# Optimization experiments

Measured on AMD Instinct MI355X. Metric: run time of the kernel, lower is better.

The kernel has to match this reference:

```python
import jax, jax.numpy as jnp
import numpy as np

B, NQ, NKV, D, H, E, FF = 2, 1024, 2048, 1024, 16, 8, 4096
DH = D // H


def _ln(x, g, b):
    m = x.mean(-1, keepdims=True)
    v = ((x - m) ** 2).mean(-1, keepdims=True)
    return (x - m) / jnp.sqrt(v + 1e-5) * g + b


def _mha(q, kv, in_w, in_b, out_w, out_b):
    # torch nn.MultiheadAttention, batch_first=True, dropout=0 (eval)
    wq, wk, wv = jnp.split(in_w, 3, axis=0)   # each [D, D]
    bq, bk, bv = jnp.split(in_b, 3)
    qp = q @ wq.T + bq
    kp = kv @ wk.T + bk
    vp = kv @ wv.T + bv

    def heads(x):
        b, t, _ = x.shape
        return x.reshape(b, t, H, DH).transpose(0, 2, 1, 3)  # [b,H,t,DH]

    qh, kh, vh = heads(qp), heads(kp), heads(vp)
    scores = jnp.einsum('bhqd,bhkd->bhqk', qh, kh) / jnp.sqrt(jnp.float32(DH))
    att = jax.nn.softmax(scores, axis=-1)
    o = jnp.einsum('bhqk,bhkd->bhqd', att, vh)
    o = o.transpose(0, 2, 1, 3).reshape(q.shape[0], q.shape[1], D)
    return o @ out_w.T + out_b


def _moe_token(x, rw, rb, nw, nb, w1, b1, w2, b2, top_k, key):
    # SparseMoE_token: per-token noisy top-k routing.
    logits = x @ rw.T + rb                      # [B,T,E]
    noise_logits = x @ nw.T + nb
    noise = jax.random.normal(key, logits.shape, logits.dtype) * jax.nn.softplus(noise_logits)
    noisy = logits + noise
    _, idx = jax.lax.top_k(noisy, top_k)        # [B,T,K]
    mask = jax.nn.one_hot(idx, E, dtype=noisy.dtype).sum(-2) > 0   # [B,T,E]
    probs = jax.nn.softmax(jnp.where(mask, noisy, -jnp.inf), axis=-1)
    # Dense expert compute weighted by sparse router probs (zeros for
    # non-selected experts) — math identical to masked gather/scatter.
    h = jax.nn.gelu(jnp.einsum('btd,edh->beth', x, w1) + b1[None, :, None, :],
                    approximate=False)          # [B,E,T,FF]
    eo = jnp.einsum('beth,ehd->betd', h, w2) + b2[None, :, None, :]
    return jnp.einsum('bte,betd->btd', probs, eo)


def reference(q, kv,
              ln_cq_g, ln_cq_b, ln_ckv_g, ln_ckv_b, ln_s_g, ln_s_b, ln_m_g, ln_m_b,
              ca_in_w, ca_in_b, ca_out_w, ca_out_b,
              sa_in_w, sa_in_b, sa_out_w, sa_out_b,
              moe_rw, moe_rb, moe_nw, moe_nb, moe_w1, moe_b1, moe_w2, moe_b2,
              top_k):
    key = jax.random.key(42)
    x = _mha(_ln(q, ln_cq_g, ln_cq_b), _ln(kv, ln_ckv_g, ln_ckv_b),
             ca_in_w, ca_in_b, ca_out_w, ca_out_b) + q
    xs = _ln(x, ln_s_g, ln_s_b)
    x = _mha(xs, xs, sa_in_w, sa_in_b, sa_out_w, sa_out_b) + x
    x = _moe_token(_ln(x, ln_m_g, ln_m_b), moe_rw, moe_rb, moe_nw, moe_nb,
                   moe_w1, moe_b1, moe_w2, moe_b2, top_k, key) + x
    return x


def setup_inputs() -> dict:
    key = jax.random.key(0)
    ks = jax.random.split(key, 16)
    s = 0.02
    return {
        'q':  jax.random.normal(ks[0], (B, NQ, D), jnp.float32),
        'kv': jax.random.normal(ks[1], (B, NKV, D), jnp.float32),
        'ln_cq_g': jnp.ones((D,), jnp.float32),  'ln_cq_b': jnp.zeros((D,), jnp.float32),
        'ln_ckv_g': jnp.ones((D,), jnp.float32), 'ln_ckv_b': jnp.zeros((D,), jnp.float32),
        'ln_s_g': jnp.ones((D,), jnp.float32),   'ln_s_b': jnp.zeros((D,), jnp.float32),
        'ln_m_g': jnp.ones((D,), jnp.float32),   'ln_m_b': jnp.zeros((D,), jnp.float32),
        'ca_in_w':  jax.random.normal(ks[2], (3 * D, D), jnp.float32) * s,
        'ca_in_b':  jnp.zeros((3 * D,), jnp.float32),
        'ca_out_w': jax.random.normal(ks[3], (D, D), jnp.float32) * s,
        'ca_out_b': jnp.zeros((D,), jnp.float32),
        'sa_in_w':  jax.random.normal(ks[4], (3 * D, D), jnp.float32) * s,
        'sa_in_b':  jnp.zeros((3 * D,), jnp.float32),
        'sa_out_w': jax.random.normal(ks[5], (D, D), jnp.float32) * s,
        'sa_out_b': jnp.zeros((D,), jnp.float32),
        'moe_rw': jax.random.normal(ks[6], (E, D), jnp.float32) * s,
        'moe_rb': jnp.zeros((E,), jnp.float32),
        'moe_nw': jax.random.normal(ks[7], (E, D), jnp.float32) * s,
        'moe_nb': jnp.zeros((E,), jnp.float32),
        'moe_w1': jax.random.normal(ks[8], (E, D, FF), jnp.float32) * s,
        'moe_b1': jnp.zeros((E, FF), jnp.float32),
        'moe_w2': jax.random.normal(ks[9], (E, FF, D), jnp.float32) * s,
        'moe_b2': jnp.zeros((E, D), jnp.float32),
        'top_k': 2,
    }
```

## Files before the change

### kernel.cpp

```cpp
#include <hip/hip_runtime.h>
#include <cstdint>
#include <cstddef>

#define JAX_THREEFRY_PARTITIONABLE 1

typedef unsigned short u16;
typedef unsigned int u32;
typedef __attribute__((ext_vector_type(8))) short bf16x8;
typedef __attribute__((ext_vector_type(4))) float f32x4;

struct Ptr8 { u16* p[8]; };

struct QkvArgs {
  const u16* ah[3]; const u16* al[3];
  const u16* wh[3]; const u16* wl[3];
  const float* bias[3];
  float* c[3];
  int M[3];
};

__device__ __forceinline__ int imin_(int a, int b) { return a < b ? a : b; }

__device__ __forceinline__ u16 f2bf_(float f) {
  unsigned u = __float_as_uint(f);
  return (u16)((u + 0x7fffu + ((u >> 16) & 1u)) >> 16);
}
__device__ __forceinline__ float bf2f_(u16 h) {
  return __uint_as_float(((unsigned)h) << 16);
}

__device__ __forceinline__ void split2_(float a, float b, u32& hi, u32& lo) {
  u16 h0 = f2bf_(a), h1 = f2bf_(b);
  u16 l0 = f2bf_(a - bf2f_(h0)), l1 = f2bf_(b - bf2f_(h1));
  hi = (u32)h0 | ((u32)h1 << 16);
  lo = (u32)l0 | ((u32)l1 << 16);
}

union FragU {
  u32 w[4];
  uint4 q;
  bf16x8 v;
};

__device__ __forceinline__ unsigned rotl32_(unsigned v, int d) {
  return (v << d) | (v >> (32 - d));
}

__device__ __forceinline__ void threefry2x32_(unsigned k0, unsigned k1,
                                              unsigned x0, unsigned x1,
                                              unsigned& o0, unsigned& o1) {
  unsigned ks2 = k0 ^ k1 ^ 0x1BD11BDAu;
  x0 += k0; x1 += k1;
#define TF_R(rot) { x0 += x1; x1 = rotl32_(x1, rot); x1 ^= x0; }
  TF_R(13) TF_R(15) TF_R(26) TF_R(6)
  x0 += k1;  x1 += ks2 + 1u;
  TF_R(17) TF_R(29) TF_R(16) TF_R(24)
  x0 += ks2; x1 += k0 + 2u;
  TF_R(13) TF_R(15) TF_R(26) TF_R(6)
  x0 += k0;  x1 += k1 + 3u;
  TF_R(17) TF_R(29) TF_R(16) TF_R(24)
  x0 += k1;  x1 += ks2 + 4u;
  TF_R(13) TF_R(15) TF_R(26) TF_R(6)
  x0 += ks2; x1 += k0 + 5u;
#undef TF_R
  o0 = x0; o1 = x1;
}

__device__ float erfinv_f32_(float x) {
  float w = -log1pf(-x * x);
  float p;
  if (w < 5.0f) {
    w -= 2.5f;
    p = 2.81022636e-08f;
    p = fmaf(p, w, 3.43273939e-07f);
    p = fmaf(p, w, -3.5233877e-06f);
    p = fmaf(p, w, -4.39150654e-06f);
    p = fmaf(p, w, 0.00021858087f);
    p = fmaf(p, w, -0.00125372503f);
    p = fmaf(p, w, -0.00417768164f);
    p = fmaf(p, w, 0.246640727f);
    p = fmaf(p, w, 1.50140941f);
  } else {
    w = sqrtf(w) - 3.0f;
    p = -0.000200214257f;
    p = fmaf(p, w, 0.000100950558f);
    p = fmaf(p, w, 0.00134934322f);
    p = fmaf(p, w, -0.00367342844f);
    p = fmaf(p, w, 0.00573950773f);
    p = fmaf(p, w, -0.0076224613f);
    p = fmaf(p, w, 0.00943887047f);
    p = fmaf(p, w, 1.00167406f);
    p = fmaf(p, w, 2.83297682f);
  }
  return p * x;
}

__device__ float bits_to_normal_(unsigned b) {
  const float lo = -0.99999994f;
  float f = __uint_as_float((b >> 9) | 0x3f800000u) - 1.0f;
  float u = fmaxf(lo, f * 2.0f + lo);
  return 1.41421356237f * erfinv_f32_(u);
}

__global__ __launch_bounds__(256) void noise_kernel(float* __restrict__ normals) {
  int i = blockIdx.x * 256 + threadIdx.x;
#if JAX_THREEFRY_PARTITIONABLE
  if (i < 16384) {
    unsigned o0, o1;
    threefry2x32_(0u, 42u, 0u, (unsigned)i, o0, o1);
    normals[i] = bits_to_normal_(o0 ^ o1);
  }
#else
  if (i < 8192) {
    unsigned o0, o1;
    threefry2x32_(0u, 42u, (unsigned)i, (unsigned)(i + 8192), o0, o1);
    normals[i] = bits_to_normal_(o0);
    normals[i + 8192] = bits_to_normal_(o1);
  }
#endif
}

__device__ float block_reduce_sum_(float v) {
  for (int m = 1; m <= 32; m <<= 1) v += __shfl_xor(v, m, 64);
  __shared__ float red[4];
  int lane = threadIdx.x & 63, w = threadIdx.x >> 6;
  if (lane == 0) red[w] = v;
  __syncthreads();
  v = red[0] + red[1] + red[2] + red[3];
  __syncthreads();
  return v;
}

__global__ __launch_bounds__(256) void ln_kernel(
    const float* __restrict__ X, const float* __restrict__ g,
    const float* __restrict__ bta, float* __restrict__ Y) {
  int row = blockIdx.x;
  int t = threadIdx.x;
  const float4* xr = (const float4*)(X + (size_t)row * 1024);
  float4 v = xr[t];
  float s = v.x + v.y + v.z + v.w;
  s = block_reduce_sum_(s);
  float mean = s * (1.0f / 1024.0f);
  float dx = v.x - mean, dy = v.y - mean, dz = v.z - mean, dw = v.w - mean;
  float sq = dx * dx + dy * dy + dz * dz + dw * dw;
  sq = block_reduce_sum_(sq);
  float rstd = 1.0f / sqrtf(sq * (1.0f / 1024.0f) + 1e-5f);
  float4 gv = ((const float4*)g)[t];
  float4 bv = ((const float4*)bta)[t];
  float4 y;
  y.x = dx * rstd * gv.x + bv.x;
  y.y = dy * rstd * gv.y + bv.y;
  y.z = dz * rstd * gv.z + bv.z;
  y.w = dw * rstd * gv.w + bv.w;
  ((float4*)(Y + (size_t)row * 1024))[t] = y;
}

__global__ __launch_bounds__(256) void ln_split_kernel(
    const float* __restrict__ X, const float* __restrict__ g,
    const float* __restrict__ bta, u16* __restrict__ Yh,
    u16* __restrict__ Yl) {
  int row = blockIdx.x;
  int t = threadIdx.x;
  const float4* xr = (const float4*)(X + (size_t)row * 1024);
  float4 v = xr[t];
  float s = v.x + v.y + v.z + v.w;
  s = block_reduce_sum_(s);
  float mean = s * (1.0f / 1024.0f);
  float dx = v.x - mean, dy = v.y - mean, dz = v.z - mean, dw = v.w - mean;
  float sq = dx * dx + dy * dy + dz * dz + dw * dw;
  sq = block_reduce_sum_(sq);
  float rstd = 1.0f / sqrtf(sq * (1.0f / 1024.0f) + 1e-5f);
  float4 gv = ((const float4*)g)[t];
  float4 bv = ((const float4*)bta)[t];
  float y[4];
  y[0] = dx * rstd * gv.x + bv.x;
  y[1] = dy * rstd * gv.y + bv.y;
  y[2] = dz * rstd * gv.z + bv.z;
  y[3] = dw * rstd * gv.w + bv.w;
  ushort4 h, l;
  u16* hp = (u16*)&h; u16* lp = (u16*)&l;
#pragma unroll
  for (int j = 0; j < 4; ++j) {
    u16 hh = f2bf_(y[j]);
    hp[j] = hh;
    lp[j] = f2bf_(y[j] - bf2f_(hh));
  }
  *(ushort4*)(Yh + (size_t)row * 1024 + t * 4) = h;
  *(ushort4*)(Yl + (size_t)row * 1024 + t * 4) = l;
}

__global__ __launch_bounds__(256) void cvt_split_kernel(
    const float* __restrict__ src, u16* __restrict__ hi,
    u16* __restrict__ lo) {
  int i = (blockIdx.x * 256 + threadIdx.x) * 4;
  float4 v = *(const float4*)(src + i);
  float a[4] = {v.x, v.y, v.z, v.w};
  ushort4 h, l;
  u16* hp = (u16*)&h; u16* lp = (u16*)&l;
#pragma unroll
  for (int j = 0; j < 4; ++j) {
    u16 hh = f2bf_(a[j]);
    hp[j] = hh;
    lp[j] = f2bf_(a[j] - bf2f_(hh));
  }
  *(ushort4*)(hi + i) = h;
  *(ushort4*)(lo + i) = l;
}

__global__ __launch_bounds__(256) void tcvt_kernel(
    const float* __restrict__ src, Ptr8 dst, int R, int C) {
  __shared__ float tile[64][65];
  const int e = blockIdx.z;
  const float* S = src + (size_t)e * R * C;
  u16* D = dst.p[e];
  const int c0 = blockIdx.x * 64, r0 = blockIdx.y * 64;
  const int t = threadIdx.x;
  const int tr = t >> 4, tc = (t & 15) * 4;
#pragma unroll
  for (int p = 0; p < 4; ++p) {
    float4 v = *(const float4*)(S + (size_t)(r0 + p * 16 + tr) * C + c0 + tc);
    tile[p * 16 + tr][tc + 0] = v.x;
    tile[p * 16 + tr][tc + 1] = v.y;
    tile[p * 16 + tr][tc + 2] = v.z;
    tile[p * 16 + tr][tc + 3] = v.w;
  }
  __syncthreads();
#pragma unroll
  for (int p = 0; p < 4; ++p) {
    int oc = p * 16 + tr;
    ushort4 o;
    o.x = f2bf_(tile[tc + 0][oc]);
    o.y = f2bf_(tile[tc + 1][oc]);
    o.z = f2bf_(tile[tc + 2][oc]);
    o.w = f2bf_(tile[tc + 3][oc]);
    *(ushort4*)(D + (size_t)(c0 + oc) * R + r0 + tc) = o;
  }
}

template<bool RESID>
__device__ __forceinline__ void split_gemm_body_(
    const u16* __restrict__ Ah, const u16* __restrict__ Al,
    const u16* __restrict__ Wh, const u16* __restrict__ Wl,
    const float* __restrict__ bias, const float* __restrict__ resid,
    float* __restrict__ C, int m0, int n0, int N, int K) {
  __shared__ __align__(16) u16 Ahs[128 * 40];
  __shared__ __align__(16) u16 Als[128 * 40];
  __shared__ __align__(16) u16 Bhs[128 * 40];
  __shared__ __align__(16) u16 Bls[128 * 40];
  const int t = threadIdx.x;
  const int lane = t & 63, wv = t >> 6;
  const int wm = (wv & 1) * 64, wn = (wv >> 1) * 64;
  const int col = lane & 15, quad = lane >> 4;
  f32x4 acc[4][4] = {};
  const int r = t >> 1, kh = (t & 1) * 16;
  const u16* pah = Ah + (size_t)(m0 + r) * K + kh;
  const u16* pal = Al + (size_t)(m0 + r) * K + kh;
  const u16* pwh = Wh + (size_t)(n0 + r) * K + kh;
  const u16* pwl = Wl + (size_t)(n0 + r) * K + kh;
  uint4 ra0 = *(const uint4*)(pah), ra1 = *(const uint4*)(pah + 8);
  uint4 rb0 = *(const uint4*)(pal), rb1 = *(const uint4*)(pal + 8);
  uint4 rc0 = *(const uint4*)(pwh), rc1 = *(const uint4*)(pwh + 8);
  uint4 rd0 = *(const uint4*)(pwl), rd1 = *(const uint4*)(pwl + 8);
  for (int k0 = 0; k0 < K; k0 += 32) {
    pah += 32; pal += 32; pwh += 32; pwl += 32;
    *(uint4*)&Ahs[r * 40 + kh] = ra0; *(uint4*)&Ahs[r * 40 + kh + 8] = ra1;
    *(uint4*)&Als[r * 40 + kh] = rb0; *(uint4*)&Als[r * 40 + kh + 8] = rb1;
    *(uint4*)&Bhs[r * 40 + kh] = rc0; *(uint4*)&Bhs[r * 40 + kh + 8] = rc1;
    *(uint4*)&Bls[r * 40 + kh] = rd0; *(uint4*)&Bls[r * 40 + kh + 8] = rd1;
    __syncthreads();
    if (k0 + 32 < K) {
      ra0 = *(const uint4*)(pah); ra1 = *(const uint4*)(pah + 8);
      rb0 = *(const uint4*)(pal); rb1 = *(const uint4*)(pal + 8);
      rc0 = *(const uint4*)(pwh); rc1 = *(const uint4*)(pwh + 8);
      rd0 = *(const uint4*)(pwl); rd1 = *(const uint4*)(pwl + 8);
    }
    bf16x8 afh[4], afl[4], bfh[4], bfl[4];
#pragma unroll
    for (int i = 0; i < 4; ++i) {
      afh[i] = *(const bf16x8*)&Ahs[(wm + i * 16 + col) * 40 + quad * 8];
      afl[i] = *(const bf16x8*)&Als[(wm + i * 16 + col) * 40 + quad * 8];
    }
#pragma unroll
    for (int j = 0; j < 4; ++j) {
      bfh[j] = *(const bf16x8*)&Bhs[(wn + j * 16 + col) * 40 + quad * 8];
      bfl[j] = *(const bf16x8*)&Bls[(wn + j * 16 + col) * 40 + quad * 8];
    }
#pragma unroll
    for (int i = 0; i < 4; ++i) {
#pragma unroll
      for (int j = 0; j < 4; ++j) {
        acc[i][j] = __builtin_amdgcn_mfma_f32_16x16x32_bf16(afh[i], bfh[j], acc[i][j], 0, 0, 0);
        acc[i][j] = __builtin_amdgcn_mfma_f32_16x16x32_bf16(afh[i], bfl[j], acc[i][j], 0, 0, 0);
        acc[i][j] = __builtin_amdgcn_mfma_f32_16x16x32_bf16(afl[i], bfh[j], acc[i][j], 0, 0, 0);
      }
    }
    __syncthreads();
  }
  float bv[4];
#pragma unroll
  for (int j = 0; j < 4; ++j) bv[j] = bias[n0 + wn + j * 16 + col];
#pragma unroll
  for (int i = 0; i < 4; ++i) {
#pragma unroll
    for (int rr = 0; rr < 4; ++rr) {
      int m = m0 + wm + i * 16 + quad * 4 + rr;
      float* crow = C + (size_t)m * N;
      const float* rrow = RESID ? (resid + (size_t)m * N) : nullptr;
#pragma unroll
      for (int j = 0; j < 4; ++j) {
        int n = n0 + wn + j * 16 + col;
        float v = acc[i][j][rr] + bv[j];
        if (RESID) v += rrow[n];
        crow[n] = v;
      }
    }
  }
}

template<bool RESID>
__global__ __launch_bounds__(256) void split_gemm_nt(
    const u16* __restrict__ Ah, const u16* __restrict__ Al,
    const u16* __restrict__ Wh, const u16* __restrict__ Wl,
    const float* __restrict__ bias, const float* __restrict__ resid,
    float* __restrict__ C, int M, int N, int K) {
  (void)M;
  split_gemm_body_<RESID>(Ah, Al, Wh, Wl, bias, resid, C,
                          blockIdx.y * 128, blockIdx.x * 128, N, K);
}

__global__ __launch_bounds__(256) void split_gemm_qkv(QkvArgs a, int N, int K) {
  const int z = blockIdx.z;
  const int m0 = blockIdx.y * 128;
  if (m0 >= a.M[z]) return;
  split_gemm_body_<false>(a.ah[z], a.al[z], a.wh[z], a.wl[z], a.bias[z],
                          nullptr, a.c[z], m0, blockIdx.x * 128, N, K);
}

__global__ __launch_bounds__(256) void attn_kernel(
    const float* __restrict__ QP, const float* __restrict__ KP,
    const float* __restrict__ VP, u16* __restrict__ AOh,
    u16* __restrict__ AOl, int nq, int nkv) {
  __shared__ __align__(16) u16 Ksh[64 * 72];
  __shared__ __align__(16) u16 Ksl[64 * 72];
  __shared__ __align__(16) u16 Vth[64 * 72];
  __shared__ __align__(16) u16 Vtl[64 * 72];
  const int t = threadIdx.x;
  const int lane = t & 63, wv = t >> 6;
  const int col = lane & 15, quad = lane >> 4;
  const int bh = blockIdx.x;
  const int b = bh >> 4, h = bh & 15;
  const int q0 = blockIdx.y * 64;
  const int wq0 = wv * 16;

  bf16x8 qbh[2], qbl[2];
  {
    const float* qsrc =
        QP + (size_t)(b * nq + q0 + wq0 + col) * 1024 + h * 64 + quad * 8;
#pragma unroll
    for (int ks = 0; ks < 2; ++ks) {
      float4 f0 = *(const float4*)(qsrc + ks * 32);
      float4 f1 = *(const float4*)(qsrc + ks * 32 + 4);
      float qf[8] = {f0.x, f0.y, f0.z, f0.w, f1.x, f1.y, f1.z, f1.w};
      FragU uh, ul;
#pragma unroll
      for (int w = 0; w < 4; ++w)
        split2_(qf[2 * w] * 0.125f, qf[2 * w + 1] * 0.125f, uh.w[w], ul.w[w]);
      qbh[ks] = uh.v;
      qbl[ks] = ul.v;
    }
  }

  f32x4 o[4] = {};
  float mi = -INFINITY, li = 0.0f;

  const int kr = t >> 2, kc = (t & 3) * 16;
  const int vg = t >> 5, vr = (t & 31) * 2;

  for (int kv0 = 0; kv0 < nkv; kv0 += 64) {
    {
      const float* ksrc =
          KP + (size_t)(b * nkv + kv0 + kr) * 1024 + h * 64 + kc;
      float4 f0 = *(const float4*)(ksrc);
      float4 f1 = *(const float4*)(ksrc + 4);
      float4 f2 = *(const float4*)(ksrc + 8);
      float4 f3 = *(const float4*)(ksrc + 12);
      float kf[16] = {f0.x, f0.y, f0.z, f0.w, f1.x, f1.y, f1.z, f1.w,
                      f2.x, f2.y, f2.z, f2.w, f3.x, f3.y, f3.z, f3.w};
      FragU h0, h1, l0, l1;
#pragma unroll
      for (int w = 0; w < 4; ++w) {
        split2_(kf[2 * w], kf[2 * w + 1], h0.w[w], l0.w[w]);
        split2_(kf[8 + 2 * w], kf[9 + 2 * w], h1.w[w], l1.w[w]);
      }
      *(uint4*)&Ksh[kr * 72 + kc] = h0.q;
      *(uint4*)&Ksh[kr * 72 + kc + 8] = h1.q;
      *(uint4*)&Ksl[kr * 72 + kc] = l0.q;
      *(uint4*)&Ksl[kr * 72 + kc + 8] = l1.q;
    }
    {
      const float* vsrc =
          VP + (size_t)(b * nkv + kv0 + vr) * 1024 + h * 64 + vg * 8;
      float4 a0 = *(const float4*)(vsrc);
      float4 a1 = *(const float4*)(vsrc + 4);
      float4 b0 = *(const float4*)(vsrc + 1024);
      float4 b1 = *(const float4*)(vsrc + 1028);
      float va[8] = {a0.x, a0.y, a0.z, a0.w, a1.x, a1.y, a1.z, a1.w};
      float vb[8] = {b0.x, b0.y, b0.z, b0.w, b1.x, b1.y, b1.z, b1.w};
#pragma unroll
      for (int e = 0; e < 8; ++e) {
        u32 hh, ll;
        split2_(va[e], vb[e], hh, ll);
        *(u32*)&Vth[(vg * 8 + e) * 72 + vr] = hh;
        *(u32*)&Vtl[(vg * 8 + e) * 72 + vr] = ll;
      }
    }
    __syncthreads();

    f32x4 st[4] = {};
#pragma unroll
    for (int ks = 0; ks < 2; ++ks) {
      bf16x8 kah[4], kal[4];
#pragma unroll
      for (int i = 0; i < 4; ++i) {
        kah[i] = *(const bf16x8*)&Ksh[(i * 16 + col) * 72 + ks * 32 + quad * 8];
        kal[i] = *(const bf16x8*)&Ksl[(i * 16 + col) * 72 + ks * 32 + quad * 8];
      }
#pragma unroll
      for (int i = 0; i < 4; ++i) {
        st[i] = __builtin_amdgcn_mfma_f32_16x16x32_bf16(kah[i], qbh[ks], st[i], 0, 0, 0);
        st[i] = __builtin_amdgcn_mfma_f32_16x16x32_bf16(kah[i], qbl[ks], st[i], 0, 0, 0);
        st[i] = __builtin_amdgcn_mfma_f32_16x16x32_bf16(kal[i], qbh[ks], st[i], 0, 0, 0);
      }
    }

    float tmax = st[0][0];
#pragma unroll
    for (int i = 0; i < 4; ++i)
#pragma unroll
      for (int r = 0; r < 4; ++r) tmax = fmaxf(tmax, st[i][r]);
    tmax = fmaxf(tmax, __shfl_xor(tmax, 16, 64));
    tmax = fmaxf(tmax, __shfl_xor(tmax, 32, 64));
    float mnew = fmaxf(mi, tmax);
    float alpha = __expf(mi - mnew);
    float tsum = 0.0f;
#pragma unroll
    for (int i = 0; i < 4; ++i) {
#pragma unroll
      for (int r = 0; r < 4; ++r) {
        float p = __expf(st[i][r] - mnew);
        st[i][r] = p;
        tsum += p;
      }
    }
    tsum += __shfl_xor(tsum, 16, 64);
    tsum += __shfl_xor(tsum, 32, 64);
    li = li * alpha + tsum;
    mi = mnew;
    float alr[4];
#pragma unroll
    for (int r = 0; r < 4; ++r)
      alr[r] = __shfl(alpha, (lane & 48) | (quad * 4 + r), 64);
#pragma unroll
    for (int j = 0; j < 4; ++j)
#pragma unroll
      for (int r = 0; r < 4; ++r) o[j][r] *= alr[r];

    u32 pkh[4][2], pkl[4][2];
#pragma unroll
    for (int i = 0; i < 4; ++i)
#pragma unroll
      for (int w = 0; w < 2; ++w)
        split2_(st[i][2 * w], st[i][2 * w + 1], pkh[i][w], pkl[i][w]);
    u32 APh[2][4], APl[2][4];
    const int par = quad >> 1;
#pragma unroll
    for (int i = 0; i < 4; ++i) {
#pragma unroll
      for (int w01 = 0; w01 < 2; ++w01) {
#pragma unroll
        for (int dw = 0; dw < 2; ++dw) {
          int src = (((2 * quad + dw) & 3) << 4) | col;
          u32 vh = (u32)__shfl((int)pkh[i][w01], src, 64);
          u32 vl = (u32)__shfl((int)pkl[i][w01], src, 64);
          if ((i & 1) == par) {
            APh[i >> 1][dw * 2 + w01] = vh;
            APl[i >> 1][dw * 2 + w01] = vl;
          }
        }
      }
    }

#pragma unroll
    for (int ks = 0; ks < 2; ++ks) {
      FragU fh, fl;
#pragma unroll
      for (int w = 0; w < 4; ++w) { fh.w[w] = APh[ks][w]; fl.w[w] = APl[ks][w]; }
      bf16x8 pah = fh.v, pal = fl.v;
#pragma unroll
      for (int j = 0; j < 4; ++j) {
        bf16x8 vbh = *(const bf16x8*)&Vth[(j * 16 + col) * 72 + ks * 32 + quad * 8];
        bf16x8 vbl = *(const bf16x8*)&Vtl[(j * 16 + col) * 72 + ks * 32 + quad * 8];
        o[j] = __builtin_amdgcn_mfma_f32_16x16x32_bf16(pah, vbh, o[j], 0, 0, 0);
        o[j] = __builtin_amdgcn_mfma_f32_16x16x32_bf16(pah, vbl, o[j], 0, 0, 0);
        o[j] = __builtin_amdgcn_mfma_f32_16x16x32_bf16(pal, vbh, o[j], 0, 0, 0);
      }
    }
    __syncthreads();
  }

  float inv = 1.0f / li;
  float ivr[4];
#pragma unroll
  for (int r = 0; r < 4; ++r)
    ivr[r] = __shfl(inv, (lane & 48) | (quad * 4 + r), 64);
#pragma unroll
  for (int r = 0; r < 4; ++r) {
    size_t base =
        (size_t)(b * nq + q0 + wq0 + quad * 4 + r) * 1024 + h * 64 + col;
#pragma unroll
    for (int j = 0; j < 4; ++j) {
      float v = o[j][r] * ivr[r];
      u16 hh = f2bf_(v);
      AOh[base + j * 16] = hh;
      AOl[base + j * 16] = f2bf_(v - bf2f_(hh));
    }
  }
}

__global__ __launch_bounds__(256) void router_kernel(
    const float* __restrict__ xm, const float* __restrict__ rw,
    const float* __restrict__ rb, const float* __restrict__ nw,
    const float* __restrict__ nb, float* __restrict__ logits,
    float* __restrict__ nlogits) {
  int row = blockIdx.x, t = threadIdx.x;
  const float* x = xm + (size_t)row * 1024;
  float accl[8] = {}, accn[8] = {};
  for (int d = t; d < 1024; d += 256) {
    float xv = x[d];
#pragma unroll
    for (int e = 0; e < 8; ++e) {
      accl[e] += xv * rw[e * 1024 + d];
      accn[e] += xv * nw[e * 1024 + d];
    }
  }
  __shared__ float red[16][4];
  int lane = t & 63, w = t >> 6;
#pragma unroll
  for (int e = 0; e < 8; ++e) {
    float v = accl[e];
    for (int m = 1; m <= 32; m <<= 1) v += __shfl_xor(v, m, 64);
    if (lane == 0) red[e][w] = v;
    float v2 = accn[e];
    for (int m = 1; m <= 32; m <<= 1) v2 += __shfl_xor(v2, m, 64);
    if (lane == 0) red[8 + e][w] = v2;
  }
  __syncthreads();
  if (t < 8)
    logits[row * 8 + t] = red[t][0] + red[t][1] + red[t][2] + red[t][3] + rb[t];
  else if (t < 16)
    nlogits[row * 8 + t - 8] =
        red[t][0] + red[t][1] + red[t][2] + red[t][3] + nb[t - 8];
}

__global__ __launch_bounds__(256) void route_kernel(
    const float* __restrict__ logits, const float* __restrict__ nlogits,
    const float* __restrict__ normals, int* __restrict__ routei,
    float* __restrict__ routep, int* __restrict__ cnt) {
  int bt = blockIdx.x * 256 + threadIdx.x;
  if (bt >= 2048) return;
  float noisy[8];
#pragma unroll
  for (int e = 0; e < 8; ++e) {
    float nl = nlogits[bt * 8 + e];
    float sp = fmaxf(nl, 0.0f) + log1pf(expf(-fabsf(nl)));
    noisy[e] = logits[bt * 8 + e] + normals[bt * 8 + e] * sp;
  }
  int i1 = 0; float n1 = noisy[0];
#pragma unroll
  for (int e = 1; e < 8; ++e) if (noisy[e] > n1) { n1 = noisy[e]; i1 = e; }
  int i2 = -1; float n2 = -INFINITY;
#pragma unroll
  for (int e = 0; e < 8; ++e)
    if (e != i1 && noisy[e] > n2) { n2 = noisy[e]; i2 = e; }
  float e2 = expf(n2 - n1);
  float denom = 1.0f + e2;
  routei[bt * 2 + 0] = i1; routei[bt * 2 + 1] = i2;
  routep[bt * 2 + 0] = 1.0f / denom; routep[bt * 2 + 1] = e2 / denom;
  atomicAdd(&cnt[i1], 1);
  atomicAdd(&cnt[i2], 1);
}

__global__ void zero_kernel(int* __restrict__ cnt) {
  if (threadIdx.x < 8) cnt[threadIdx.x] = 0;
}

__global__ void offs_kernel(const int* __restrict__ cnt, int* __restrict__ offs,
                            int* __restrict__ fill) {
  if (threadIdx.x == 0 && blockIdx.x == 0) {
    int o = 0;
    for (int e = 0; e < 8; ++e) { offs[e] = o; o += cnt[e]; fill[e] = 0; }
  }
}

__global__ __launch_bounds__(256) void fill_kernel(
    const int* __restrict__ routei, const float* __restrict__ routep,
    const int* __restrict__ offs, int* __restrict__ fill,
    int* __restrict__ alist, float* __restrict__ aprob) {
  int bt = blockIdx.x * 256 + threadIdx.x;
  if (bt >= 2048) return;
#pragma unroll
  for (int s = 0; s < 2; ++s) {
    int e = routei[bt * 2 + s];
    int pos = offs[e] + atomicAdd(&fill[e], 1);
    alist[pos] = bt;
    aprob[pos] = routep[bt * 2 + s];
  }
}

__global__ __launch_bounds__(256) void copy_kernel(const float* __restrict__ src,
                                                   float* __restrict__ dst) {
  int i = blockIdx.x * 256 + threadIdx.x;
  ((float4*)dst)[i] = ((const float4*)src)[i];
}

__global__ __launch_bounds__(256) void f2bf_kernel(const float* __restrict__ src,
                                                   u16* __restrict__ dst) {
  int i = (blockIdx.x * 256 + threadIdx.x) * 4;
  float4 v = *(const float4*)(src + i);
  ushort4 o;
  o.x = f2bf_(v.x); o.y = f2bf_(v.y); o.z = f2bf_(v.z); o.w = f2bf_(v.w);
  *(ushort4*)(dst + i) = o;
}

__device__ __forceinline__ float gelu_exact_(float x) {
  return 0.5f * x * (1.0f + erff(x * 0.70710678f));
}

__global__ __launch_bounds__(256) void ffn1_mfma(
    const u16* __restrict__ Xb, Ptr8 w1t, const float* __restrict__ B1,
    u16* __restrict__ H, const int* __restrict__ alist,
    const int* __restrict__ cnt, const int* __restrict__ offs) {
  const int e = blockIdx.z;
  const int ce = cnt[e];
  const int m0 = blockIdx.y * 128;
  if (m0 >= ce) return;
  const int off = offs[e];
  const int n0 = blockIdx.x * 128;
  const u16* __restrict__ WT = w1t.p[e];
  __shared__ __align__(16) u16 As[128 * 40];
  __shared__ __align__(16) u16 Bs[128 * 40];
  const int t = threadIdx.x;
  const int lane = t & 63, wv = t >> 6;
  const int wm = (wv & 1) * 64, wn = (wv >> 1) * 64;
  const int col = lane & 15, quad = lane >> 4;
  f32x4 acc[4][4] = {};
  const int r = t >> 1, ak = (t & 1) * 16;
  const int arow = alist[off + imin_(m0 + r, ce - 1)];
  const u16* asrc = Xb + (size_t)arow * 1024 + ak;
  const u16* wsrc = WT + (size_t)(n0 + r) * 1024 + ak;
  uint4 ra0 = *(const uint4*)(asrc), ra1 = *(const uint4*)(asrc + 8);
  uint4 rb0 = *(const uint4*)(wsrc), rb1 = *(const uint4*)(wsrc + 8);
  for (int k0 = 0; k0 < 1024; k0 += 32) {
    asrc += 32; wsrc += 32;
    *(uint4*)&As[r * 40 + ak] = ra0; *(uint4*)&As[r * 40 + ak + 8] = ra1;
    *(uint4*)&Bs[r * 40 + ak] = rb0; *(uint4*)&Bs[r * 40 + ak + 8] = rb1;
    __syncthreads();
    if (k0 + 32 < 1024) {
      ra0 = *(const uint4*)(asrc); ra1 = *(const uint4*)(asrc + 8);
      rb0 = *(const uint4*)(wsrc); rb1 = *(const uint4*)(wsrc + 8);
    }
    bf16x8 af[4], bf[4];
#pragma unroll
    for (int i = 0; i < 4; ++i)
      af[i] = *(const bf16x8*)&As[(wm + i * 16 + col) * 40 + quad * 8];
#pragma unroll
    for (int j = 0; j < 4; ++j)
      bf[j] = *(const bf16x8*)&Bs[(wn + j * 16 + col) * 40 + quad * 8];
#pragma unroll
    for (int i = 0; i < 4; ++i)
#pragma unroll
      for (int j = 0; j < 4; ++j)
        acc[i][j] = __builtin_amdgcn_mfma_f32_16x16x32_bf16(af[i], bf[j], acc[i][j], 0, 0, 0);
    __syncthreads();
  }
#pragma unroll
  for (int j = 0; j < 4; ++j) {
    int n = n0 + wn + j * 16 + col;
    float bv = B1[(size_t)e * 4096 + n];
#pragma unroll
    for (int i = 0; i < 4; ++i) {
#pragma unroll
      for (int r2 = 0; r2 < 4; ++r2) {
        int m = m0 + wm + i * 16 + quad * 4 + r2;
        if (m < ce) {
          float v = gelu_exact_(acc[i][j][r2] + bv);
          H[(size_t)(off + m) * 4096 + n] = f2bf_(v);
        }
      }
    }
  }
}

__global__ __launch_bounds__(256) void ffn2_mfma(
    const u16* __restrict__ H, Ptr8 w2t, const float* __restrict__ B2,
    float* __restrict__ Out, const int* __restrict__ alist,
    const float* __restrict__ aprob, const int* __restrict__ cnt,
    const int* __restrict__ offs) {
  const int e = blockIdx.z;
  const int ce = cnt[e];
  const int mt = blockIdx.y >> 2, ks = blockIdx.y & 3;
  const int m0 = mt * 128;
  if (m0 >= ce) return;
  const int off = offs[e];
  const int n0 = blockIdx.x * 128;
  const u16* __restrict__ WT = w2t.p[e];
  __shared__ __align__(16) u16 As[128 * 40];
  __shared__ __align__(16) u16 Bs[128 * 40];
  const int t = threadIdx.x;
  const int lane = t & 63, wv = t >> 6;
  const int wm = (wv & 1) * 64, wn = (wv >> 1) * 64;
  const int col = lane & 15, quad = lane >> 4;
  f32x4 acc[4][4] = {};
  const int r = t >> 1, ak = (t & 1) * 16;
  const u16* asrc =
      H + (size_t)(off + imin_(m0 + r, ce - 1)) * 4096 + ks * 1024 + ak;
  const u16* wsrc = WT + (size_t)(n0 + r) * 4096 + ks * 1024 + ak;
  uint4 ra0 = *(const uint4*)(asrc), ra1 = *(const uint4*)(asrc + 8);
  uint4 rb0 = *(const uint4*)(wsrc), rb1 = *(const uint4*)(wsrc + 8);
  for (int k0 = 0; k0 < 1024; k0 += 32) {
    asrc += 32; wsrc += 32;
    *(uint4*)&As[r * 40 + ak] = ra0; *(uint4*)&As[r * 40 + ak + 8] = ra1;
    *(uint4*)&Bs[r * 40 + ak] = rb0; *(uint4*)&Bs[r * 40 + ak + 8] = rb1;
    __syncthreads();
    if (k0 + 32 < 1024) {
      ra0 = *(const uint4*)(asrc); ra1 = *(const uint4*)(asrc + 8);
      rb0 = *(const uint4*)(wsrc); rb1 = *(const uint4*)(wsrc + 8);
    }
    bf16x8 af[4], bf[4];
#pragma unroll
    for (int i = 0; i < 4; ++i)
      af[i] = *(const bf16x8*)&As[(wm + i * 16 + col) * 40 + quad * 8];
#pragma unroll
    for (int j = 0; j < 4; ++j)
      bf[j] = *(const bf16x8*)&Bs[(wn + j * 16 + col) * 40 + quad * 8];
#pragma unroll
    for (int i = 0; i < 4; ++i)
#pragma unroll
      for (int j = 0; j < 4; ++j)
        acc[i][j] = __builtin_amdgcn_mfma_f32_16x16x32_bf16(af[i], bf[j], acc[i][j], 0, 0, 0);
    __syncthreads();
  }
  float bv[4];
#pragma unroll
  for (int j = 0; j < 4; ++j)
    bv[j] = (ks == 0) ? B2[(size_t)e * 1024 + n0 + wn + j * 16 + col] : 0.0f;
#pragma unroll
  for (int i = 0; i < 4; ++i) {
#pragma unroll
    for (int r2 = 0; r2 < 4; ++r2) {
      int m = m0 + wm + i * 16 + quad * 4 + r2;
      if (m < ce) {
        int aidx = off + m;
        int tok = alist[aidx];
        float p = aprob[aidx];
        float* orow = Out + (size_t)tok * 1024;
#pragma unroll
        for (int j = 0; j < 4; ++j) {
          int n = n0 + wn + j * 16 + col;
          atomicAdd(&orow[n], p * (acc[i][j][r2] + bv[j]));
        }
      }
    }
  }
}

extern "C" void kernel_launch(void* const* d_in, const int* in_sizes, int n_in,
                              void* d_out, int out_size, void* d_ws, size_t ws_size,
                              hipStream_t stream) {
  (void)in_sizes; (void)n_in; (void)out_size; (void)ws_size;
  const float* q        = (const float*)d_in[0];
  const float* kv       = (const float*)d_in[1];
  const float* ln_cq_g  = (const float*)d_in[2];
  const float* ln_cq_b  = (const float*)d_in[3];
  const float* ln_ckv_g = (const float*)d_in[4];
  const float* ln_ckv_b = (const float*)d_in[5];
  const float* ln_s_g   = (const float*)d_in[6];
  const float* ln_s_b   = (const float*)d_in[7];
  const float* ln_m_g   = (const float*)d_in[8];
  const float* ln_m_b   = (const float*)d_in[9];
  const float* ca_in_w  = (const float*)d_in[10];
  const float* ca_in_b  = (const float*)d_in[11];
  const float* ca_out_w = (const float*)d_in[12];
  const float* ca_out_b = (const float*)d_in[13];
  const float* sa_in_w  = (const float*)d_in[14];
  const float* sa_in_b  = (const float*)d_in[15];
  const float* sa_out_w = (const float*)d_in[16];
  const float* sa_out_b = (const float*)d_in[17];
  const float* moe_rw   = (const float*)d_in[18];
  const float* moe_rb   = (const float*)d_in[19];
  const float* moe_nw   = (const float*)d_in[20];
  const float* moe_nb   = (const float*)d_in[21];
  const float* moe_w1   = (const float*)d_in[22];
  const float* moe_b1   = (const float*)d_in[23];
  const float* moe_w2   = (const float*)d_in[24];
  const float* moe_b2   = (const float*)d_in[25];
  float* out = (float*)d_out;

  float* ws = (float*)d_ws;
  const size_t MEG = 1u << 20;
  float* x1   = ws;
  float* x2   = ws + 2 * MEG;
  float* xm   = ws + 4 * MEG;
  u16*   aoh  = (u16*)(ws + 6 * MEG);
  u16*   aol  = (u16*)(ws + 7 * MEG);
  float* misc = ws + 8 * MEG;
  float* normals = misc;
  float* logits  = misc + 16384;
  float* nlogits = misc + 32768;
  float* routep  = misc + 49152;
  float* aprob   = misc + 53248;
  int*   routei  = (int*)(misc + 57344);
  int*   alist   = (int*)(misc + 61440);
  int*   cnt     = (int*)(misc + 65536);
  int*   offs    = cnt + 8;
  int*   fillc   = cnt + 16;
  float* RA = ws + 8 * MEG + 131072;
  u16*   w1h = (u16*)RA;
  u16*   w1l = (u16*)(RA + (3 * MEG) / 2);
  u16*   w2h = (u16*)(RA + 3 * MEG);
  u16*   w2l = (u16*)(RA + 3 * MEG + MEG / 2);
  u16*   a1h = (u16*)(RA + 4 * MEG);
  u16*   a1l = (u16*)(RA + 5 * MEG);
  u16*   a2h = (u16*)(RA + 6 * MEG);
  u16*   a2l = (u16*)(RA + 8 * MEG);
  float* qp  = RA + 10 * MEG;
  float* kp  = RA + 12 * MEG;
  float* vp  = RA + 16 * MEG;
  u16*   xb  = (u16*)RA;
  u16*   hb  = (u16*)(RA + 1 * MEG);
  Ptr8 wt;
  wt.p[0] = (u16*)(RA + 9 * MEG);
  wt.p[1] = (u16*)(RA + 11 * MEG);
  wt.p[2] = (u16*)(RA + 13 * MEG);
  wt.p[3] = (u16*)(RA + 15 * MEG);
  wt.p[4] = (u16*)(RA + 17 * MEG);
  wt.p[5] = (u16*)x1;
  wt.p[6] = (u16*)xm;
  wt.p[7] = (u16*)(ws + 6 * MEG);

  dim3 blk(256);

  zero_kernel<<<dim3(1), blk, 0, stream>>>(cnt);
  noise_kernel<<<dim3(64), blk, 0, stream>>>(normals);

  cvt_split_kernel<<<dim3(3072), blk, 0, stream>>>(ca_in_w, w1h, w1l);
  cvt_split_kernel<<<dim3(1024), blk, 0, stream>>>(ca_out_w, w2h, w2l);
  ln_split_kernel<<<dim3(2048), blk, 0, stream>>>(q, ln_cq_g, ln_cq_b, a1h, a1l);
  ln_split_kernel<<<dim3(4096), blk, 0, stream>>>(kv, ln_ckv_g, ln_ckv_b, a2h, a2l);
  {
    QkvArgs qa;
    qa.ah[0] = a1h; qa.al[0] = a1l;
    qa.ah[1] = a2h; qa.al[1] = a2l;
    qa.ah[2] = a2h; qa.al[2] = a2l;
    for (int z = 0; z < 3; ++z) {
      qa.wh[z] = w1h + (size_t)z * MEG;
      qa.wl[z] = w1l + (size_t)z * MEG;
      qa.bias[z] = ca_in_b + z * 1024;
    }
    qa.c[0] = qp; qa.c[1] = kp; qa.c[2] = vp;
    qa.M[0] = 2048; qa.M[1] = 4096; qa.M[2] = 4096;
    split_gemm_qkv<<<dim3(8, 32, 3), blk, 0, stream>>>(qa, 1024, 1024);
  }
  attn_kernel<<<dim3(32, 16), blk, 0, stream>>>(qp, kp, vp, aoh, aol, 1024, 2048);
  split_gemm_nt<true><<<dim3(8, 16), blk, 0, stream>>>(
      aoh, aol, w2h, w2l, ca_out_b, q, x1, 2048, 1024, 1024);

  cvt_split_kernel<<<dim3(3072), blk, 0, stream>>>(sa_in_w, w1h, w1l);
  cvt_split_kernel<<<dim3(1024), blk, 0, stream>>>(sa_out_w, w2h, w2l);
  ln_split_kernel<<<dim3(2048), blk, 0, stream>>>(x1, ln_s_g, ln_s_b, a1h, a1l);
  {
    QkvArgs qa;
    for (int z = 0; z < 3; ++z) {
      qa.ah[z] = a1h; qa.al[z] = a1l;
      qa.wh[z] = w1h + (size_t)z * MEG;
      qa.wl[z] = w1l + (size_t)z * MEG;
      qa.bias[z] = sa_in_b + z * 1024;
      qa.M[z] = 2048;
    }
    qa.c[0] = qp; qa.c[1] = kp; qa.c[2] = vp;
    split_gemm_qkv<<<dim3(8, 16, 3), blk, 0, stream>>>(qa, 1024, 1024);
  }
  attn_kernel<<<dim3(32, 16), blk, 0, stream>>>(qp, kp, vp, aoh, aol, 1024, 1024);
  split_gemm_nt<true><<<dim3(8, 16), blk, 0, stream>>>(
      aoh, aol, w2h, w2l, sa_out_b, x1, x2, 2048, 1024, 1024);

  ln_kernel<<<dim3(2048), blk, 0, stream>>>(x2, ln_m_g, ln_m_b, xm);
  f2bf_kernel<<<dim3(2048), blk, 0, stream>>>(xm, xb);
  router_kernel<<<dim3(2048), blk, 0, stream>>>(xm, moe_rw, moe_rb, moe_nw, moe_nb, logits, nlogits);
  route_kernel<<<dim3(8), blk, 0, stream>>>(logits, nlogits, normals, routei, routep, cnt);
  offs_kernel<<<dim3(1), blk, 0, stream>>>(cnt, offs, fillc);
  fill_kernel<<<dim3(8), blk, 0, stream>>>(routei, routep, offs, fillc, alist, aprob);
  copy_kernel<<<dim3(2048), blk, 0, stream>>>(x2, out);
  tcvt_kernel<<<dim3(64, 16, 8), blk, 0, stream>>>(moe_w1, wt, 1024, 4096);
  ffn1_mfma<<<dim3(32, 16, 8), blk, 0, stream>>>(xb, wt, moe_b1, hb, alist, cnt, offs);
  tcvt_kernel<<<dim3(16, 64, 8), blk, 0, stream>>>(moe_w2, wt, 4096, 1024);
  ffn2_mfma<<<dim3(8, 64, 8), blk, 0, stream>>>(hb, wt, moe_b2, out, alist, aprob, cnt, offs);
}
```

Measured before the change: 1.067 ms.

## Load GEMM tiles directly into LDS with global_load_lds in three kernels

The split-precision GEMM and both MoE FFN kernels now stage A/B tiles with direct global-to-LDS 16-byte loads instead of register prefetch followed by LDS stores. The LDS row stride drops from 40 to 32 halves to fit the contiguous layout that the direct loads require. This removes register staging and the explicit LDS writes. In exchange, the register-level software prefetch overlap is gone, since loads are now issued and waited on in the same iteration. The unpadded stride may also cause LDS bank conflicts on the fragment reads.

```diff
diff --git a/kernel.cpp b/kernel.cpp
--- a/kernel.cpp
+++ b/kernel.cpp
@@ -20,6 +20,12 @@
 };
 
 __device__ __forceinline__ int imin_(int a, int b) { return a < b ? a : b; }
+
+__device__ __forceinline__ void gl16_(const void* g, void* l) {
+  __builtin_amdgcn_global_load_lds(
+      (const __attribute__((address_space(1))) void*)g,
+      (__attribute__((address_space(3))) void*)l, 16, 0, 0);
+}
 
 __device__ __forceinline__ u16 f2bf_(float f) {
   unsigned u = __float_as_uint(f);
@@ -243,47 +249,46 @@
     const u16* __restrict__ Wh, const u16* __restrict__ Wl,
     const float* __restrict__ bias, const float* __restrict__ resid,
     float* __restrict__ C, int m0, int n0, int N, int K) {
-  __shared__ __align__(16) u16 Ahs[128 * 40];
-  __shared__ __align__(16) u16 Als[128 * 40];
-  __shared__ __align__(16) u16 Bhs[128 * 40];
-  __shared__ __align__(16) u16 Bls[128 * 40];
+  __shared__ __align__(16) u16 Ahs[128 * 32];
+  __shared__ __align__(16) u16 Als[128 * 32];
+  __shared__ __align__(16) u16 Bhs[128 * 32];
+  __shared__ __align__(16) u16 Bls[128 * 32];
   const int t = threadIdx.x;
   const int lane = t & 63, wv = t >> 6;
   const int wm = (wv & 1) * 64, wn = (wv >> 1) * 64;
   const int col = lane & 15, quad = lane >> 4;
   f32x4 acc[4][4] = {};
-  const int r = t >> 1, kh = (t & 1) * 16;
-  const u16* pah = Ah + (size_t)(m0 + r) * K + kh;
-  const u16* pal = Al + (size_t)(m0 + r) * K + kh;
-  const u16* pwh = Wh + (size_t)(n0 + r) * K + kh;
-  const u16* pwl = Wl + (size_t)(n0 + r) * K + kh;
-  uint4 ra0 = *(const uint4*)(pah), ra1 = *(const uint4*)(pah + 8);
-  uint4 rb0 = *(const uint4*)(pal), rb1 = *(const uint4*)(pal + 8);
-  uint4 rc0 = *(const uint4*)(pwh), rc1 = *(const uint4*)(pwh + 8);
-  uint4 rd0 = *(const uint4*)(pwl), rd1 = *(const uint4*)(pwl + 8);
+  const int r0 = t >> 2, kq = (t & 3) * 8;
+  const u16* pah0 = Ah + (size_t)(m0 + r0) * K + kq;
+  const u16* pah1 = Ah + (size_t)(m0 + r0 + 64) * K + kq;
+  const u16* pal0 = Al + (size_t)(m0 + r0) * K + kq;
+  const u16* pal1 = Al + (size_t)(m0 + r0 + 64) * K + kq;
+  const u16* pwh0 = Wh + (size_t)(n0 + r0) * K + kq;
+  const u16* pwh1 = Wh + (size_t)(n0 + r0 + 64) * K + kq;
+  const u16* pwl0 = Wl + (size_t)(n0 + r0) * K + kq;
+  const u16* pwl1 = Wl + (size_t)(n0 + r0 + 64) * K + kq;
+  u16* lah0 = &Ahs[t * 8];       u16* lah1 = &Ahs[(t + 256) * 8];
+  u16* lal0 = &Als[t * 8];       u16* lal1 = &Als[(t + 256) * 8];
+  u16* lbh0 = &Bhs[t * 8];       u16* lbh1 = &Bhs[(t + 256) * 8];
+  u16* lbl0 = &Bls[t * 8];       u16* lbl1 = &Bls[(t + 256) * 8];
   for (int k0 = 0; k0 < K; k0 += 32) {
-    pah += 32; pal += 32; pwh += 32; pwl += 32;
-    *(uint4*)&Ahs[r * 40 + kh] = ra0; *(uint4*)&Ahs[r * 40 + kh + 8] = ra1;
-    *(uint4*)&Als[r * 40 + kh] = rb0; *(uint4*)&Als[r * 40 + kh + 8] = rb1;
-    *(uint4*)&Bhs[r * 40 + kh] = rc0; *(uint4*)&Bhs[r * 40 + kh + 8] = rc1;
-    *(uint4*)&Bls[r * 40 + kh] = rd0; *(uint4*)&Bls[r * 40 + kh + 8] = rd1;
+    gl16_(pah0, lah0); gl16_(pah1, lah1);
+    gl16_(pal0, lal0); gl16_(pal1, lal1);
+    gl16_(pwh0, lbh0); gl16_(pwh1, lbh1);
+    gl16_(pwl0, lbl0); gl16_(pwl1, lbl1);
+    pah0 += 32; pah1 += 32; pal0 += 32; pal1 += 32;
+    pwh0 += 32; pwh1 += 32; pwl0 += 32; pwl1 += 32;
     __syncthreads();
-    if (k0 + 32 < K) {
-      ra0 = *(const uint4*)(pah); ra1 = *(const uint4*)(pah + 8);
-      rb0 = *(const uint4*)(pal); rb1 = *(const uint4*)(pal + 8);
-      rc0 = *(const uint4*)(pwh); rc1 = *(const uint4*)(pwh + 8);
-      rd0 = *(const uint4*)(pwl); rd1 = *(const uint4*)(pwl + 8);
-    }
     bf16x8 afh[4], afl[4], bfh[4], bfl[4];
 #pragma unroll
     for (int i = 0; i < 4; ++i) {
-      afh[i] = *(const bf16x8*)&Ahs[(wm + i * 16 + col) * 40 + quad * 8];
-      afl[i] = *(const bf16x8*)&Als[(wm + i * 16 + col) * 40 + quad * 8];
+      afh[i] = *(const bf16x8*)&Ahs[(wm + i * 16 + col) * 32 + quad * 8];
+      afl[i] = *(const bf16x8*)&Als[(wm + i * 16 + col) * 32 + quad * 8];
     }
 #pragma unroll
     for (int j = 0; j < 4; ++j) {
-      bfh[j] = *(const bf16x8*)&Bhs[(wn + j * 16 + col) * 40 + quad * 8];
-      bfl[j] = *(const bf16x8*)&Bls[(wn + j * 16 + col) * 40 + quad * 8];
+      bfh[j] = *(const bf16x8*)&Bhs[(wn + j * 16 + col) * 32 + quad * 8];
+      bfl[j] = *(const bf16x8*)&Bls[(wn + j * 16 + col) * 32 + quad * 8];
     }
 #pragma unroll
     for (int i = 0; i < 4; ++i) {
@@ -647,35 +652,34 @@
   const int off = offs[e];
   const int n0 = blockIdx.x * 128;
   const u16* __restrict__ WT = w1t.p[e];
-  __shared__ __align__(16) u16 As[128 * 40];
-  __shared__ __align__(16) u16 Bs[128 * 40];
+  __shared__ __align__(16) u16 As[128 * 32];
+  __shared__ __align__(16) u16 Bs[128 * 32];
   const int t = threadIdx.x;
   const int lane = t & 63, wv = t >> 6;
   const int wm = (wv & 1) * 64, wn = (wv >> 1) * 64;
   const int col = lane & 15, quad = lane >> 4;
   f32x4 acc[4][4] = {};
-  const int r = t >> 1, ak = (t & 1) * 16;
-  const int arow = alist[off + imin_(m0 + r, ce - 1)];
-  const u16* asrc = Xb + (size_t)arow * 1024 + ak;
-  const u16* wsrc = WT + (size_t)(n0 + r) * 1024 + ak;
-  uint4 ra0 = *(const uint4*)(asrc), ra1 = *(const uint4*)(asrc + 8);
-  uint4 rb0 = *(const uint4*)(wsrc), rb1 = *(const uint4*)(wsrc + 8);
+  const int r0 = t >> 2, kq = (t & 3) * 8;
+  const int arow0 = alist[off + imin_(m0 + r0, ce - 1)];
+  const int arow1 = alist[off + imin_(m0 + r0 + 64, ce - 1)];
+  const u16* pa0 = Xb + (size_t)arow0 * 1024 + kq;
+  const u16* pa1 = Xb + (size_t)arow1 * 1024 + kq;
+  const u16* pw0 = WT + (size_t)(n0 + r0) * 1024 + kq;
+  const u16* pw1 = WT + (size_t)(n0 + r0 + 64) * 1024 + kq;
+  u16* la0 = &As[t * 8]; u16* la1 = &As[(t + 256) * 8];
+  u16* lb0 = &Bs[t * 8]; u16* lb1 = &Bs[(t + 256) * 8];
   for (int k0 = 0; k0 < 1024; k0 += 32) {
-    asrc += 32; wsrc += 32;
-    *(uint4*)&As[r * 40 + ak] = ra0; *(uint4*)&As[r * 40 + ak + 8] = ra1;
-    *(uint4*)&Bs[r * 40 + ak] = rb0; *(uint4*)&Bs[r * 40 + ak + 8] = rb1;
+    gl16_(pa0, la0); gl16_(pa1, la1);
+    gl16_(pw0, lb0); gl16_(pw1, lb1);
+    pa0 += 32; pa1 += 32; pw0 += 32; pw1 += 32;
     __syncthreads();
-    if (k0 + 32 < 1024) {
-      ra0 = *(const uint4*)(asrc); ra1 = *(const uint4*)(asrc + 8);
-      rb0 = *(const uint4*)(wsrc); rb1 = *(const uint4*)(wsrc + 8);
-    }
     bf16x8 af[4], bf[4];
 #pragma unroll
     for (int i = 0; i < 4; ++i)
-      af[i] = *(const bf16x8*)&As[(wm + i * 16 + col) * 40 + quad * 8];
+      af[i] = *(const bf16x8*)&As[(wm + i * 16 + col) * 32 + quad * 8];
 #pragma unroll
     for (int j = 0; j < 4; ++j)
-      bf[j] = *(const bf16x8*)&Bs[(wn + j * 16 + col) * 40 + quad * 8];
+      bf[j] = *(const bf16x8*)&Bs[(wn + j * 16 + col) * 32 + quad * 8];
 #pragma unroll
     for (int i = 0; i < 4; ++i)
 #pragma unroll
@@ -714,35 +718,34 @@
   const int off = offs[e];
   const int n0 = blockIdx.x * 128;
   const u16* __restrict__ WT = w2t.p[e];
-  __shared__ __align__(16) u16 As[128 * 40];
-  __shared__ __align__(16) u16 Bs[128 * 40];
+  __shared__ __align__(16) u16 As[128 * 32];
+  __shared__ __align__(16) u16 Bs[128 * 32];
   const int t = threadIdx.x;
   const int lane = t & 63, wv = t >> 6;
   const int wm = (wv & 1) * 64, wn = (wv >> 1) * 64;
   const int col = lane & 15, quad = lane >> 4;
   f32x4 acc[4][4] = {};
-  const int r = t >> 1, ak = (t & 1) * 16;
-  const u16* asrc =
-      H + (size_t)(off + imin_(m0 + r, ce - 1)) * 4096 + ks * 1024 + ak;
-  const u16* wsrc = WT + (size_t)(n0 + r) * 4096 + ks * 1024 + ak;
-  uint4 ra0 = *(const uint4*)(asrc), ra1 = *(const uint4*)(asrc + 8);
-  uint4 rb0 = *(const uint4*)(wsrc), rb1 = *(const uint4*)(wsrc + 8);
+  const int r0 = t >> 2, kq = (t & 3) * 8;
+  const u16* pa0 =
+      H + (size_t)(off + imin_(m0 + r0, ce - 1)) * 4096 + ks * 1024 + kq;
+  const u16* pa1 =
+      H + (size_t)(off + imin_(m0 + r0 + 64, ce - 1)) * 4096 + ks * 1024 + kq;
+  const u16* pw0 = WT + (size_t)(n0 + r0) * 4096 + ks * 1024 + kq;
+  const u16* pw1 = WT + (size_t)(n0 + r0 + 64) * 4096 + ks * 1024 + kq;
+  u16* la0 = &As[t * 8]; u16* la1 = &As[(t + 256) * 8];
+  u16* lb0 = &Bs[t * 8]; u16* lb1 = &Bs[(t + 256) * 8];
   for (int k0 = 0; k0 < 1024; k0 += 32) {
-    asrc += 32; wsrc += 32;
-    *(uint4*)&As[r * 40 + ak] = ra0; *(uint4*)&As[r * 40 + ak + 8] = ra1;
-    *(uint4*)&Bs[r * 40 + ak] = rb0; *(uint4*)&Bs[r * 40 + ak + 8] = rb1;
+    gl16_(pa0, la0); gl16_(pa1, la1);
+    gl16_(pw0, lb0); gl16_(pw1, lb1);
+    pa0 += 32; pa1 += 32; pw0 += 32; pw1 += 32;
     __syncthreads();
-    if (k0 + 32 < 1024) {
-      ra0 = *(const uint4*)(asrc); ra1 = *(const uint4*)(asrc + 8);
-      rb0 = *(const uint4*)(wsrc); rb1 = *(const uint4*)(wsrc + 8);
-    }
     bf16x8 af[4], bf[4];
 #pragma unroll
     for (int i = 0; i < 4; ++i)
-      af[i] = *(const bf16x8*)&As[(wm + i * 16 + col) * 40 + quad * 8];
+      af[i] = *(const bf16x8*)&As[(wm + i * 16 + col) * 32 + quad * 8];
 #pragma unroll
     for (int j = 0; j < 4; ++j)
-      bf[j] = *(const bf16x8*)&Bs[(wn + j * 16 + col) * 40 + quad * 8];
+      bf[j] = *(const bf16x8*)&Bs[(wn + j * 16 + col) * 32 + quad * 8];
 #pragma unroll
     for (int i = 0; i < 4; ++i)
 #pragma unroll
```

New measurement: 1.069 ms. About the same (+0.2%).
